# Optimization experiments

Measured on AMD Instinct MI355X. Metric: run time of the kernel, lower is better.

## Reference

```python
import jax, jax.numpy as jnp
import numpy as np

D_MODEL = 2048
N_HEADS = 16
HEAD_DIM = D_MODEL // N_HEADS  # 128
B, S = 4, 2048


def setup_inputs() -> dict:
    key = jax.random.key(0)
    ks = jax.random.split(key, 7)
    scale = 1.0 / np.sqrt(D_MODEL)
    return {
        "x": jax.random.normal(ks[0], (B, S, D_MODEL), dtype=jnp.float32),
        "cos": jax.random.uniform(ks[1], (S, HEAD_DIM // 2), dtype=jnp.float32),
        "sin": jax.random.uniform(ks[2], (S, HEAD_DIM // 2), dtype=jnp.float32),
        "Wq": jax.random.normal(ks[3], (D_MODEL, D_MODEL), dtype=jnp.float32) * scale,
        "Wk": jax.random.normal(ks[4], (D_MODEL, D_MODEL), dtype=jnp.float32) * scale,
        "Wv": jax.random.normal(ks[5], (D_MODEL, D_MODEL), dtype=jnp.float32) * scale,
        "Wo": jax.random.normal(ks[6], (D_MODEL, D_MODEL), dtype=jnp.float32) * scale,
    }


def apply_rope(x, cos, sin):
    # x: [B, H, S, head_dim]; cos/sin: [S, half] (split-in-half RoPE)
    half = x.shape[-1] // 2
    x1, x2 = x[..., :half], x[..., half:]
    cos = cos[None, None, :, :].astype(x.dtype)
    sin = sin[None, None, :, :].astype(x.dtype)
    return jnp.concatenate([x1 * cos - x2 * sin, x1 * sin + x2 * cos], axis=-1)


def reference(x, cos, sin, Wq, Wk, Wv, Wo):
    Bx, Sx, _ = x.shape
    # nn.Linear: y = x @ W.T
    def proj(W):
        y = jnp.einsum("bsd,ed->bse", x, W)
        return y.reshape(Bx, Sx, N_HEADS, HEAD_DIM).transpose(0, 2, 1, 3)  # [B,H,S,hd]
    q = apply_rope(proj(Wq), cos, sin)
    k = apply_rope(proj(Wk), cos, sin)
    v = proj(Wv)
    scale = 1.0 / np.sqrt(HEAD_DIM)
    scores = jnp.einsum("bhqd,bhkd->bhqk", q, k) * scale  # [B,H,S,S]
    attn = jax.nn.softmax(scores, axis=-1)
    out = jnp.einsum("bhqk,bhkd->bhqd", attn, v)
    out = out.transpose(0, 2, 1, 3).reshape(Bx, Sx, D_MODEL)
    return jnp.einsum("bsd,ed->bse", out, Wo)
```

## Files before the change

### kernel.cpp

```cpp
#include <hip/hip_runtime.h>

typedef _Float16 half_t;
typedef __attribute__((ext_vector_type(8))) _Float16 half8;
typedef __attribute__((ext_vector_type(4))) _Float16 half4v;
typedef __attribute__((ext_vector_type(4))) float f32x4;

#define MFMA16(a,b,c) __builtin_amdgcn_mfma_f32_16x16x32_f16((a),(b),(c),0,0,0)

__device__ __forceinline__ void gld_lds16(const half_t* g, half_t* l){
    __builtin_amdgcn_global_load_lds((__attribute__((address_space(1))) void*)(g),
                                     (__attribute__((address_space(3))) void*)(l), 16, 0, 0);
}

__global__ __launch_bounds__(256) void cvt_k(const float* __restrict__ s, half_t* __restrict__ d, int n4){
    int i = blockIdx.x * 256 + threadIdx.x;
    if (i < n4){
        float4 v = ((const float4*)s)[i];
        half4v h = { (half_t)v.x, (half_t)v.y, (half_t)v.z, (half_t)v.w };
        ((half4v*)d)[i] = h;
    }
}

__global__ __launch_bounds__(256) void gemm_nt(const half_t* __restrict__ A, const half_t* __restrict__ B,
                                               half_t* __restrict__ Qw, half_t* __restrict__ Kw,
                                               half_t* __restrict__ Vt, float* __restrict__ Co, int kind){
    const int tid  = threadIdx.x;
    const int lane = tid & 63;
    const int wav  = tid >> 6;
    const int wm   = (wav >> 1) * 64;
    const int wn   = (wav & 1) * 64;
    const int bm   = blockIdx.x;
    const int bn   = blockIdx.y;
    const int KD   = 2048;

    __shared__ __align__(16) half_t As[128*64];
    __shared__ __align__(16) half_t Bs[128*64];

    f32x4 acc[4][4] = {};

    const half_t* Ab = A + (size_t)bm * 128 * KD;
    const half_t* Bb = B + (size_t)bn * 128 * KD;

    for (int k0 = 0; k0 < KD; k0 += 64){
#pragma unroll
        for (int i = 0; i < 4; i++){
            int c = tid + i*256;
            gld_lds16(Ab + (size_t)(c>>3)*KD + k0 + (c&7)*8, As + c*8);
        }
#pragma unroll
        for (int i = 0; i < 4; i++){
            int c = tid + i*256;
            gld_lds16(Bb + (size_t)(c>>3)*KD + k0 + (c&7)*8, Bs + c*8);
        }
        __syncthreads();
#pragma unroll
        for (int ks = 0; ks < 2; ks++){
            const int kb = ks*32 + (lane>>4)*8;
            half8 af[4], bf[4];
#pragma unroll
            for (int mi = 0; mi < 4; mi++) af[mi] = *(const half8*)(As + (wm + mi*16 + (lane&15))*64 + kb);
#pragma unroll
            for (int ni = 0; ni < 4; ni++) bf[ni] = *(const half8*)(Bs + (wn + ni*16 + (lane&15))*64 + kb);
#pragma unroll
            for (int mi = 0; mi < 4; mi++)
#pragma unroll
                for (int ni = 0; ni < 4; ni++)
                    acc[mi][ni] = MFMA16(af[mi], bf[ni], acc[mi][ni]);
        }
        __syncthreads();
    }

    const int rbase = wm + (lane>>4)*4;
    const int cbase = wn + (lane&15);

    if (kind == 0){
        const int which = bn >> 4;
        const int nb = (bn & 15) * 128;
        if (which < 2){
            half_t* dst = which ? Kw : Qw;
#pragma unroll
            for (int mi = 0; mi < 4; mi++)
#pragma unroll
                for (int ni = 0; ni < 4; ni++)
#pragma unroll
                    for (int r = 0; r < 4; r++){
                        int m = bm*128 + rbase + mi*16 + r;
                        int n = nb + cbase + ni*16;
                        dst[(((size_t)(m>>11)*16 + (n>>7))*2048 + (m&2047))*128 + (n&127)] = (half_t)acc[mi][ni][r];
                    }
        } else {
#pragma unroll
            for (int mi = 0; mi < 4; mi++)
#pragma unroll
                for (int ni = 0; ni < 4; ni++){
                    int m0 = bm*128 + rbase + mi*16;
                    int n  = nb + cbase + ni*16;
                    half4v h = {(half_t)acc[mi][ni][0], (half_t)acc[mi][ni][1],
                                (half_t)acc[mi][ni][2], (half_t)acc[mi][ni][3]};
                    *(half4v*)(Vt + (((size_t)(m0>>11)*16 + (n>>7))*128 + (n&127))*2048 + (m0&2047)) = h;
                }
        }
    } else {
#pragma unroll
        for (int mi = 0; mi < 4; mi++)
#pragma unroll
            for (int ni = 0; ni < 4; ni++)
#pragma unroll
                for (int r = 0; r < 4; r++){
                    int m = bm*128 + rbase + mi*16 + r;
                    int n = bn*128 + cbase + ni*16;
                    Co[(size_t)m*2048 + n] = acc[mi][ni][r];
                }
    }
}

__global__ __launch_bounds__(256) void rope_k(half_t* __restrict__ Qw, half_t* __restrict__ Kw,
                                              const float* __restrict__ cs, const float* __restrict__ sn){
    int t  = blockIdx.x * 256 + threadIdx.x;
    int d  = t & 63;
    int s  = (t >> 6) & 2047;
    int bh = t >> 17;
    float c  = cs[s*64 + d];
    float si = sn[s*64 + d];
    size_t base = ((size_t)bh*2048 + s)*128 + d;
    float q1 = (float)Qw[base], q2 = (float)Qw[base+64];
    Qw[base]    = (half_t)(q1*c - q2*si);
    Qw[base+64] = (half_t)(q1*si + q2*c);
    float k1 = (float)Kw[base], k2 = (float)Kw[base+64];
    Kw[base]    = (half_t)(k1*c - k2*si);
    Kw[base+64] = (half_t)(k1*si + k2*c);
}

__global__ __launch_bounds__(256) void attn_k(const half_t* __restrict__ Q, const half_t* __restrict__ K,
                                              const half_t* __restrict__ Vt, half_t* __restrict__ AO){
    const int tid  = threadIdx.x;
    const int lane = tid & 63;
    const int w    = lane >> 4;
    const int l15  = lane & 15;
    const int l7   = lane & 7;
    const int wav  = tid >> 6;
    const int qt   = blockIdx.x;
    const int bh   = blockIdx.y;

    __shared__ __align__(16) half_t smem[8192 + 8192 + 4*2560];
    half_t* Ks = smem;
    half_t* Vs = smem + 8192;
    half_t* Ps = smem + 16384 + wav*2560;
    half_t* Ob = smem + wav*4096;

    const half_t* Qb = Q + ((size_t)bh*2048 + qt*128 + wav*32)*128;
    half8 aq[2][4];
#pragma unroll
    for (int qi = 0; qi < 2; qi++)
#pragma unroll
        for (int ks = 0; ks < 4; ks++)
            aq[qi][ks] = *(const half8*)(Qb + (qi*16 + l15)*128 + ks*32 + w*8);

    f32x4 oacc[8][2] = {};
    float m_[2] = {-1e30f, -1e30f};
    float l_[2] = {0.0f, 0.0f};

    const float SSC = 0.08838834764831845f * 1.4426950408889634f;

    for (int kt = 0; kt < 32; kt++){
        const half_t* Kb = K  + ((size_t)bh*2048 + kt*64)*128;
        const half_t* Vb = Vt + (size_t)bh*128*2048 + kt*64;
        __syncthreads();
#pragma unroll
        for (int i = 0; i < 4; i++){
            int c = tid + i*256;
            int key = c >> 4, pc = c & 15;
            gld_lds16(Kb + key*128 + ((pc ^ (key&7)) << 3), Ks + c*8);
        }
#pragma unroll
        for (int i = 0; i < 4; i++){
            int c = tid + i*256;
            int d = c >> 3, pc = c & 7;
            gld_lds16(Vb + (size_t)d*2048 + ((pc ^ (d&7)) << 3), Vs + c*8);
        }
        __syncthreads();

        f32x4 sacc[4][2] = {};
#pragma unroll
        for (int ks = 0; ks < 4; ks++){
            half8 kf[4];
#pragma unroll
            for (int t = 0; t < 4; t++){
                int key = t*16 + l15;
                kf[t] = *(const half8*)(Ks + key*128 + (((ks*4 + w) ^ l7) << 3));
            }
#pragma unroll
            for (int t = 0; t < 4; t++)
#pragma unroll
                for (int qi = 0; qi < 2; qi++)
                    sacc[t][qi] = MFMA16(kf[t], aq[qi][ks], sacc[t][qi]);
        }

#pragma unroll
        for (int qi = 0; qi < 2; qi++){
            float mx = sacc[0][qi][0];
#pragma unroll
            for (int t = 0; t < 4; t++)
#pragma unroll
                for (int r = 0; r < 4; r++) mx = fmaxf(mx, sacc[t][qi][r]);
            mx = fmaxf(mx, __shfl_xor(mx, 16));
            mx = fmaxf(mx, __shfl_xor(mx, 32));
            float mn = fmaxf(m_[qi], mx*SSC);
            float alpha = exp2f(m_[qi] - mn);
            m_[qi] = mn;
            float sum = 0.0f;
#pragma unroll
            for (int t = 0; t < 4; t++){
                float p0 = exp2f(sacc[t][qi][0]*SSC - mn);
                float p1 = exp2f(sacc[t][qi][1]*SSC - mn);
                float p2 = exp2f(sacc[t][qi][2]*SSC - mn);
                float p3 = exp2f(sacc[t][qi][3]*SSC - mn);
                sum += (p0 + p1) + (p2 + p3);
                half4v h = {(half_t)p0, (half_t)p1, (half_t)p2, (half_t)p3};
                *(half4v*)(Ps + (qi*16 + l15)*80 + t*16 + w*4) = h;
            }
            sum += __shfl_xor(sum, 16);
            sum += __shfl_xor(sum, 32);
            l_[qi] = l_[qi]*alpha + sum;
#pragma unroll
            for (int t = 0; t < 8; t++)
#pragma unroll
                for (int r = 0; r < 4; r++) oacc[t][qi][r] *= alpha;
        }

#pragma unroll
        for (int c2 = 0; c2 < 2; c2++){
            half8 vf[8], pf[2];
#pragma unroll
            for (int t = 0; t < 8; t++){
                int d = t*16 + l15;
                vf[t] = *(const half8*)(Vs + d*64 + (((c2*4 + w) ^ l7) << 3));
            }
#pragma unroll
            for (int qi = 0; qi < 2; qi++)
                pf[qi] = *(const half8*)(Ps + (qi*16 + l15)*80 + c2*32 + w*8);
#pragma unroll
            for (int t = 0; t < 8; t++)
#pragma unroll
                for (int qi = 0; qi < 2; qi++)
                    oacc[t][qi] = MFMA16(vf[t], pf[qi], oacc[t][qi]);
        }
    }

    float inv[2] = {1.0f / l_[0], 1.0f / l_[1]};
    __syncthreads();
#pragma unroll
    for (int t = 0; t < 8; t++)
#pragma unroll
        for (int qi = 0; qi < 2; qi++){
            int q  = qi*16 + l15;
            int c8 = t*2 + (w>>1);
            int pc = c8 ^ l7;
            half4v h = {(half_t)(oacc[t][qi][0]*inv[qi]), (half_t)(oacc[t][qi][1]*inv[qi]),
                        (half_t)(oacc[t][qi][2]*inv[qi]), (half_t)(oacc[t][qi][3]*inv[qi])};
            *(half4v*)(Ob + q*128 + pc*8 + (w&1)*4) = h;
        }
    const int b = bh >> 4, h = bh & 15;
#pragma unroll
    for (int it = 0; it < 8; it++){
        int q  = it*4 + w;
        half8 rd = *(const half8*)(Ob + q*128 + ((l15 ^ (q&7)) << 3));
        int s = qt*128 + wav*32 + q;
        *(half8*)(AO + ((size_t)b*2048 + s)*2048 + h*128 + l15*8) = rd;
    }
}

extern "C" void kernel_launch(void* const* d_in, const int* in_sizes, int n_in,
                              void* d_out, int out_size, void* d_ws, size_t ws_size,
                              hipStream_t stream){
    const float* x  = (const float*)d_in[0];
    const float* cs = (const float*)d_in[1];
    const float* sn = (const float*)d_in[2];
    const float* Wq = (const float*)d_in[3];
    const float* Wk = (const float*)d_in[4];
    const float* Wv = (const float*)d_in[5];
    const float* Wo = (const float*)d_in[6];

    half_t* ws = (half_t*)d_ws;
    half_t* xh = ws;
    half_t* w4 = ws + (size_t)16777216;
    half_t* qw = ws + (size_t)33554432;
    half_t* kw = ws + (size_t)50331648;
    half_t* vt = ws + (size_t)67108864;
    half_t* ao = ws + (size_t)83886080;

    cvt_k<<<16384, 256, 0, stream>>>(x,  xh,            4194304);
    cvt_k<<<4096,  256, 0, stream>>>(Wq, w4,            1048576);
    cvt_k<<<4096,  256, 0, stream>>>(Wk, w4 + 4194304,  1048576);
    cvt_k<<<4096,  256, 0, stream>>>(Wv, w4 + 8388608,  1048576);
    cvt_k<<<4096,  256, 0, stream>>>(Wo, w4 + 12582912, 1048576);

    gemm_nt<<<dim3(64, 48), 256, 0, stream>>>(xh, w4, qw, kw, vt, nullptr, 0);
    rope_k<<<32768, 256, 0, stream>>>(qw, kw, cs, sn);
    attn_k<<<dim3(16, 64), 256, 0, stream>>>(qw, kw, vt, ao);
    gemm_nt<<<dim3(64, 16), 256, 0, stream>>>(ao, w4 + 12582912, nullptr, nullptr, nullptr,
                                              (float*)d_out, 1);
}
```

Measured before the change: 802.8 us.

## Swizzle GEMM LDS tiles, store Q/K row-major, stage V transpose, merge weight conversions

The GEMM now XOR-swizzles its LDS tiles to cut bank conflicts on the MFMA fragment loads. Q and K are written in plain [B,S,D] layout, and rope and attention index them with a 2048 stride. The V projection transposes its tile through LDS so the global stores are coalesced 16-byte writes. The four weight conversion launches become one kernel, and attention gets a launch bound of 3 blocks plus interleaved fragment loads and MFMAs to lower register use, at some risk of spills.

```diff
diff --git a/kernel.cpp b/kernel.cpp
--- a/kernel.cpp
+++ b/kernel.cpp
@@ -21,11 +21,25 @@
     }
 }
 
+__global__ __launch_bounds__(256) void cvtw_k(const float* __restrict__ w0, const float* __restrict__ w1,
+                                              const float* __restrict__ w2, const float* __restrict__ w3,
+                                              half_t* __restrict__ dst){
+    const float* srcs[4] = {w0, w1, w2, w3};
+    const float* s = srcs[blockIdx.y];
+    int i = blockIdx.x * 256 + threadIdx.x;
+    float4 v = ((const float4*)s)[i];
+    half4v h = { (half_t)v.x, (half_t)v.y, (half_t)v.z, (half_t)v.w };
+    ((half4v*)(dst))[(size_t)blockIdx.y * 1048576 + i] = h;
+}
+
 __global__ __launch_bounds__(256) void gemm_nt(const half_t* __restrict__ A, const half_t* __restrict__ B,
                                                half_t* __restrict__ Qw, half_t* __restrict__ Kw,
                                                half_t* __restrict__ Vt, float* __restrict__ Co, int kind){
     const int tid  = threadIdx.x;
     const int lane = tid & 63;
+    const int w    = lane >> 4;
+    const int l15  = lane & 15;
+    const int l7   = lane & 7;
     const int wav  = tid >> 6;
     const int wm   = (wav >> 1) * 64;
     const int wn   = (wav & 1) * 64;
@@ -33,8 +47,9 @@
     const int bn   = blockIdx.y;
     const int KD   = 2048;
 
-    __shared__ __align__(16) half_t As[128*64];
-    __shared__ __align__(16) half_t Bs[128*64];
+    __shared__ __align__(16) half_t smem[16384];
+    half_t* As = smem;
+    half_t* Bs = smem + 8192;
 
     f32x4 acc[4][4] = {};
 
@@ -45,22 +60,25 @@
 #pragma unroll
         for (int i = 0; i < 4; i++){
             int c = tid + i*256;
-            gld_lds16(Ab + (size_t)(c>>3)*KD + k0 + (c&7)*8, As + c*8);
+            int r = c >> 3, p = c & 7;
+            gld_lds16(Ab + (size_t)r*KD + k0 + ((p ^ (r&7)) << 3), As + c*8);
         }
 #pragma unroll
         for (int i = 0; i < 4; i++){
             int c = tid + i*256;
-            gld_lds16(Bb + (size_t)(c>>3)*KD + k0 + (c&7)*8, Bs + c*8);
+            int r = c >> 3, p = c & 7;
+            gld_lds16(Bb + (size_t)r*KD + k0 + ((p ^ (r&7)) << 3), Bs + c*8);
         }
         __syncthreads();
 #pragma unroll
         for (int ks = 0; ks < 2; ks++){
-            const int kb = ks*32 + (lane>>4)*8;
             half8 af[4], bf[4];
 #pragma unroll
-            for (int mi = 0; mi < 4; mi++) af[mi] = *(const half8*)(As + (wm + mi*16 + (lane&15))*64 + kb);
-#pragma unroll
-            for (int ni = 0; ni < 4; ni++) bf[ni] = *(const half8*)(Bs + (wn + ni*16 + (lane&15))*64 + kb);
+            for (int mi = 0; mi < 4; mi++)
+                af[mi] = *(const half8*)(As + (wm + mi*16 + l15)*64 + (((ks*4 + w) ^ l7) << 3));
+#pragma unroll
+            for (int ni = 0; ni < 4; ni++)
+                bf[ni] = *(const half8*)(Bs + (wn + ni*16 + l15)*64 + (((ks*4 + w) ^ l7) << 3));
 #pragma unroll
             for (int mi = 0; mi < 4; mi++)
 #pragma unroll
@@ -70,8 +88,8 @@
         __syncthreads();
     }
 
-    const int rbase = wm + (lane>>4)*4;
-    const int cbase = wn + (lane&15);
+    const int rbase = wm + w*4;
+    const int cbase = wn + l15;
 
     if (kind == 0){
         const int which = bn >> 4;
@@ -86,19 +104,28 @@
                     for (int r = 0; r < 4; r++){
                         int m = bm*128 + rbase + mi*16 + r;
                         int n = nb + cbase + ni*16;
-                        dst[(((size_t)(m>>11)*16 + (n>>7))*2048 + (m&2047))*128 + (n&127)] = (half_t)acc[mi][ni][r];
+                        dst[(size_t)m*2048 + n] = (half_t)acc[mi][ni][r];
                     }
         } else {
 #pragma unroll
             for (int mi = 0; mi < 4; mi++)
 #pragma unroll
                 for (int ni = 0; ni < 4; ni++){
-                    int m0 = bm*128 + rbase + mi*16;
-                    int n  = nb + cbase + ni*16;
+                    int n  = cbase + ni*16;
+                    int m0 = wm + mi*16 + w*4;
                     half4v h = {(half_t)acc[mi][ni][0], (half_t)acc[mi][ni][1],
                                 (half_t)acc[mi][ni][2], (half_t)acc[mi][ni][3]};
-                    *(half4v*)(Vt + (((size_t)(m0>>11)*16 + (n>>7))*128 + (n&127))*2048 + (m0&2047)) = h;
+                    *(half4v*)(smem + n*128 + (((m0>>3) ^ (n&7)) << 3) + (m0 & 7)) = h;
                 }
+            __syncthreads();
+            const int bh = (bm >> 4)*16 + (bn & 15);
+            const int s0 = (bm & 15) * 128;
+#pragma unroll
+            for (int it = 0; it < 32; it++){
+                int d = it*4 + w;
+                half8 rd = *(const half8*)(smem + d*128 + ((l15 ^ (d&7)) << 3));
+                *(half8*)(Vt + ((size_t)bh*128 + d)*2048 + s0 + l15*8) = rd;
+            }
         }
     } else {
 #pragma unroll
@@ -116,13 +143,14 @@
 
 __global__ __launch_bounds__(256) void rope_k(half_t* __restrict__ Qw, half_t* __restrict__ Kw,
                                               const float* __restrict__ cs, const float* __restrict__ sn){
-    int t  = blockIdx.x * 256 + threadIdx.x;
-    int d  = t & 63;
-    int s  = (t >> 6) & 2047;
-    int bh = t >> 17;
+    int t = blockIdx.x * 256 + threadIdx.x;
+    int d = t & 63;
+    int h = (t >> 6) & 15;
+    int s = (t >> 10) & 2047;
+    int b = t >> 21;
     float c  = cs[s*64 + d];
     float si = sn[s*64 + d];
-    size_t base = ((size_t)bh*2048 + s)*128 + d;
+    size_t base = ((size_t)(b*2048 + s))*2048 + h*128 + d;
     float q1 = (float)Qw[base], q2 = (float)Qw[base+64];
     Qw[base]    = (half_t)(q1*c - q2*si);
     Qw[base+64] = (half_t)(q1*si + q2*c);
@@ -131,8 +159,8 @@
     Kw[base+64] = (half_t)(k1*si + k2*c);
 }
 
-__global__ __launch_bounds__(256) void attn_k(const half_t* __restrict__ Q, const half_t* __restrict__ K,
-                                              const half_t* __restrict__ Vt, half_t* __restrict__ AO){
+__global__ __launch_bounds__(256, 3) void attn_k(const half_t* __restrict__ Q, const half_t* __restrict__ K,
+                                                 const half_t* __restrict__ Vt, half_t* __restrict__ AO){
     const int tid  = threadIdx.x;
     const int lane = tid & 63;
     const int w    = lane >> 4;
@@ -141,6 +169,7 @@
     const int wav  = tid >> 6;
     const int qt   = blockIdx.x;
     const int bh   = blockIdx.y;
+    const int b    = bh >> 4, h = bh & 15;
 
     __shared__ __align__(16) half_t smem[8192 + 8192 + 4*2560];
     half_t* Ks = smem;
@@ -148,13 +177,13 @@
     half_t* Ps = smem + 16384 + wav*2560;
     half_t* Ob = smem + wav*4096;
 
-    const half_t* Qb = Q + ((size_t)bh*2048 + qt*128 + wav*32)*128;
+    const half_t* Qb = Q + ((size_t)(b*2048 + qt*128 + wav*32))*2048 + h*128;
     half8 aq[2][4];
 #pragma unroll
     for (int qi = 0; qi < 2; qi++)
 #pragma unroll
         for (int ks = 0; ks < 4; ks++)
-            aq[qi][ks] = *(const half8*)(Qb + (qi*16 + l15)*128 + ks*32 + w*8);
+            aq[qi][ks] = *(const half8*)(Qb + (size_t)(qi*16 + l15)*2048 + ks*32 + w*8);
 
     f32x4 oacc[8][2] = {};
     float m_[2] = {-1e30f, -1e30f};
@@ -163,14 +192,14 @@
     const float SSC = 0.08838834764831845f * 1.4426950408889634f;
 
     for (int kt = 0; kt < 32; kt++){
-        const half_t* Kb = K  + ((size_t)bh*2048 + kt*64)*128;
+        const half_t* Kb = K  + ((size_t)(b*2048 + kt*64))*2048 + h*128;
         const half_t* Vb = Vt + (size_t)bh*128*2048 + kt*64;
         __syncthreads();
 #pragma unroll
         for (int i = 0; i < 4; i++){
             int c = tid + i*256;
             int key = c >> 4, pc = c & 15;
-            gld_lds16(Kb + key*128 + ((pc ^ (key&7)) << 3), Ks + c*8);
+            gld_lds16(Kb + (size_t)key*2048 + ((pc ^ (key&7)) << 3), Ks + c*8);
         }
 #pragma unroll
         for (int i = 0; i < 4; i++){
@@ -183,17 +212,12 @@
         f32x4 sacc[4][2] = {};
 #pragma unroll
         for (int ks = 0; ks < 4; ks++){
-            half8 kf[4];
 #pragma unroll
             for (int t = 0; t < 4; t++){
-                int key = t*16 + l15;
-                kf[t] = *(const half8*)(Ks + key*128 + (((ks*4 + w) ^ l7) << 3));
+                half8 kf = *(const half8*)(Ks + (t*16 + l15)*128 + (((ks*4 + w) ^ l7) << 3));
+                sacc[t][0] = MFMA16(kf, aq[0][ks], sacc[t][0]);
+                sacc[t][1] = MFMA16(kf, aq[1][ks], sacc[t][1]);
             }
-#pragma unroll
-            for (int t = 0; t < 4; t++)
-#pragma unroll
-                for (int qi = 0; qi < 2; qi++)
-                    sacc[t][qi] = MFMA16(kf[t], aq[qi][ks], sacc[t][qi]);
         }
 
 #pragma unroll
@@ -216,8 +240,8 @@
                 float p2 = exp2f(sacc[t][qi][2]*SSC - mn);
                 float p3 = exp2f(sacc[t][qi][3]*SSC - mn);
                 sum += (p0 + p1) + (p2 + p3);
-                half4v h = {(half_t)p0, (half_t)p1, (half_t)p2, (half_t)p3};
-                *(half4v*)(Ps + (qi*16 + l15)*80 + t*16 + w*4) = h;
+                half4v hv = {(half_t)p0, (half_t)p1, (half_t)p2, (half_t)p3};
+                *(half4v*)(Ps + (qi*16 + l15)*80 + t*16 + w*4) = hv;
             }
             sum += __shfl_xor(sum, 16);
             sum += __shfl_xor(sum, 32);
@@ -230,20 +254,14 @@
 
 #pragma unroll
         for (int c2 = 0; c2 < 2; c2++){
-            half8 vf[8], pf[2];
+            half8 pf0 = *(const half8*)(Ps + l15*80        + c2*32 + w*8);
+            half8 pf1 = *(const half8*)(Ps + (16 + l15)*80 + c2*32 + w*8);
 #pragma unroll
             for (int t = 0; t < 8; t++){
-                int d = t*16 + l15;
-                vf[t] = *(const half8*)(Vs + d*64 + (((c2*4 + w) ^ l7) << 3));
+                half8 vf = *(const half8*)(Vs + (t*16 + l15)*64 + (((c2*4 + w) ^ l7) << 3));
+                oacc[t][0] = MFMA16(vf, pf0, oacc[t][0]);
+                oacc[t][1] = MFMA16(vf, pf1, oacc[t][1]);
             }
-#pragma unroll
-            for (int qi = 0; qi < 2; qi++)
-                pf[qi] = *(const half8*)(Ps + (qi*16 + l15)*80 + c2*32 + w*8);
-#pragma unroll
-            for (int t = 0; t < 8; t++)
-#pragma unroll
-                for (int qi = 0; qi < 2; qi++)
-                    oacc[t][qi] = MFMA16(vf[t], pf[qi], oacc[t][qi]);
         }
     }
 
@@ -256,17 +274,16 @@
             int q  = qi*16 + l15;
             int c8 = t*2 + (w>>1);
             int pc = c8 ^ l7;
-            half4v h = {(half_t)(oacc[t][qi][0]*inv[qi]), (half_t)(oacc[t][qi][1]*inv[qi]),
-                        (half_t)(oacc[t][qi][2]*inv[qi]), (half_t)(oacc[t][qi][3]*inv[qi])};
-            *(half4v*)(Ob + q*128 + pc*8 + (w&1)*4) = h;
-        }
-    const int b = bh >> 4, h = bh & 15;
+            half4v hv = {(half_t)(oacc[t][qi][0]*inv[qi]), (half_t)(oacc[t][qi][1]*inv[qi]),
+                         (half_t)(oacc[t][qi][2]*inv[qi]), (half_t)(oacc[t][qi][3]*inv[qi])};
+            *(half4v*)(Ob + q*128 + pc*8 + (w&1)*4) = hv;
+        }
 #pragma unroll
     for (int it = 0; it < 8; it++){
         int q  = it*4 + w;
         half8 rd = *(const half8*)(Ob + q*128 + ((l15 ^ (q&7)) << 3));
         int s = qt*128 + wav*32 + q;
-        *(half8*)(AO + ((size_t)b*2048 + s)*2048 + h*128 + l15*8) = rd;
+        *(half8*)(AO + ((size_t)(b*2048 + s))*2048 + h*128 + l15*8) = rd;
     }
 }
 
@@ -289,11 +306,8 @@
     half_t* vt = ws + (size_t)67108864;
     half_t* ao = ws + (size_t)83886080;
 
-    cvt_k<<<16384, 256, 0, stream>>>(x,  xh,            4194304);
-    cvt_k<<<4096,  256, 0, stream>>>(Wq, w4,            1048576);
-    cvt_k<<<4096,  256, 0, stream>>>(Wk, w4 + 4194304,  1048576);
-    cvt_k<<<4096,  256, 0, stream>>>(Wv, w4 + 8388608,  1048576);
-    cvt_k<<<4096,  256, 0, stream>>>(Wo, w4 + 12582912, 1048576);
+    cvt_k<<<16384, 256, 0, stream>>>(x, xh, 4194304);
+    cvtw_k<<<dim3(4096, 4), 256, 0, stream>>>(Wq, Wk, Wv, Wo, w4);
 
     gemm_nt<<<dim3(64, 48), 256, 0, stream>>>(xh, w4, qw, kw, vt, nullptr, 0);
     rope_k<<<32768, 256, 0, stream>>>(qw, kw, cs, sn);
```

Result: slower. 884.2 us (+10.1%).
